# Performance work log

Hardware: AMD Instinct MI355X
Metric: run time of the kernel (lower is better)

Reference implementation:

```python
import jax, jax.numpy as jnp
import numpy as np

B, S, D = 4, 2048, 1024
H = 16
DK = D // H  # 64

def setup_inputs() -> dict:
    key = jax.random.key(0)
    ks = jax.random.split(key, 5)
    scale = 0.02
    return {
        "x": jax.random.normal(ks[0], (B, S, D), dtype=jnp.float32),
        "Wq": jax.random.normal(ks[1], (D, D), dtype=jnp.float32) * scale,
        "Wk": jax.random.normal(ks[2], (D, D), dtype=jnp.float32) * scale,
        "Wv": jax.random.normal(ks[3], (D, D), dtype=jnp.float32) * scale,
        "Wo": jax.random.normal(ks[4], (D, D), dtype=jnp.float32) * scale,
    }

def reference(x, Wq, Wk, Wv, Wo):
    b, s, d = x.shape
    h, dk = H, DK
    # torch nn.Linear(bias=False): y = x @ W.T
    q = (x @ Wq.T).reshape(b, s, h, dk).transpose(0, 2, 1, 3)  # [b,h,s,dk]
    k = (x @ Wk.T).reshape(b, s, h, dk).transpose(0, 2, 1, 3)
    v = (x @ Wv.T).reshape(b, s, h, dk).transpose(0, 2, 1, 3)
    scores = jnp.einsum('bhqd,bhkd->bhqk', q, k) * (dk ** -0.5)
    causal = jnp.triu(jnp.ones((s, s), dtype=bool), k=1)  # True = masked out
    scores = jnp.where(causal, -jnp.inf, scores)
    probs = jax.nn.softmax(scores, axis=-1)
    attn = jnp.einsum('bhqk,bhkd->bhqd', probs, v)  # [b,h,s,dk]
    attn = attn.transpose(0, 2, 1, 3).reshape(b, s, d)
    return attn @ Wo.T
```

## Files before the change

kernel.cpp:

```cpp
#include <hip/hip_runtime.h>

typedef __attribute__((ext_vector_type(8))) short bf16x8;
typedef __attribute__((ext_vector_type(4))) float f32x4;
typedef __attribute__((ext_vector_type(2))) unsigned int u32x2;
typedef unsigned int u32;
typedef unsigned short u16;

constexpr int Bb = 4, S = 2048, D = 1024, H = 16, DK = 64, M = Bb * S;

#if __has_builtin(__builtin_amdgcn_exp2f)
#define EXP2F __builtin_amdgcn_exp2f
#else
#define EXP2F exp2f
#endif

__device__ __forceinline__ u16 f2bf(float f) {
  u32 u = __float_as_uint(f);
  return (u16)((u + 0x7fffu + ((u >> 16) & 1u)) >> 16);
}

__device__ __forceinline__ u32 cvt_pk_bf16(float a, float b) {
  u32 r;
  asm("v_cvt_pk_bf16_f32 %0, %1, %2" : "=v"(r) : "v"(a), "v"(b));
  return r;
}

__device__ __forceinline__ void gld_lds16(const u16* g, u16* l) {
  __builtin_amdgcn_global_load_lds((const __attribute__((address_space(1))) u32*)g,
                                   (__attribute__((address_space(3))) u32*)l, 16, 0, 0);
}

__global__ void cast_kernel(const float* __restrict__ s, u16* __restrict__ d, int n) {
  int i = (blockIdx.x * blockDim.x + threadIdx.x) * 4;
  if (i >= n) return;
  float4 f = *(const float4*)(s + i);
  ushort4 o;
  o.x = f2bf(f.x); o.y = f2bf(f.y); o.z = f2bf(f.z); o.w = f2bf(f.w);
  *(ushort4*)(d + i) = o;
}

struct CastArgs { const float* s[4]; u16* d[4]; float sc[4]; };
__global__ void cast4_kernel(CastArgs a) {
  int i = (blockIdx.x * blockDim.x + threadIdx.x) * 4;
  int w = i >> 20;
  int off = i & ((1 << 20) - 1);
  float sc = a.sc[w];
  float4 f = *(const float4*)(a.s[w] + off);
  ushort4 o;
  o.x = f2bf(f.x * sc); o.y = f2bf(f.y * sc); o.z = f2bf(f.z * sc); o.w = f2bf(f.w * sc);
  *(ushort4*)(a.d[w] + off) = o;
}

template <bool OUTF32>
__device__ __forceinline__ void gemm_core(const u16* __restrict__ A,
                                          const u16* __restrict__ Bt,
                                          float* __restrict__ Cf, u16* __restrict__ Cb,
                                          int Nn, int Kk, int m0, int n0,
                                          u16* As, u16* Bs) {
  const int tid = threadIdx.x, wave = tid >> 6, lane = tid & 63;
  const int quad = lane >> 4, col = lane & 15;
  const int wm = wave >> 1, wn = wave & 1;

  f32x4 acc[4][4];
#pragma unroll
  for (int i = 0; i < 4; i++)
#pragma unroll
    for (int j = 0; j < 4; j++) acc[i][j] = (f32x4){0.f, 0.f, 0.f, 0.f};

  for (int k0 = 0; k0 < Kk; k0 += 64) {
#pragma unroll
    for (int j = 0; j < 4; j++) {
      int g = (wave * 4 + j) * 64;
      int gl = g + lane;
      int r = gl >> 3, sl = gl & 7;
      int kof = (sl ^ (r & 7)) * 8;
      const u16* ga = A + (size_t)(m0 + r) * Kk + k0 + kof;
      gld_lds16(ga, &As[g * 8]);
      const u16* gb = Bt + (size_t)(n0 + r) * Kk + k0 + kof;
      gld_lds16(gb, &Bs[g * 8]);
    }
    __syncthreads();
#pragma unroll
    for (int kb = 0; kb < 2; kb++) {
      bf16x8 af[4], bfr[4];
#pragma unroll
      for (int mi = 0; mi < 4; mi++) {
        int R = wm * 64 + mi * 16 + col;
        af[mi] = *(const bf16x8*)&As[R * 64 + (((kb * 4 + quad) ^ (R & 7)) << 3)];
      }
#pragma unroll
      for (int ni = 0; ni < 4; ni++) {
        int R = wn * 64 + ni * 16 + col;
        bfr[ni] = *(const bf16x8*)&Bs[R * 64 + (((kb * 4 + quad) ^ (R & 7)) << 3)];
      }
#pragma unroll
      for (int mi = 0; mi < 4; mi++)
#pragma unroll
        for (int ni = 0; ni < 4; ni++)
          acc[mi][ni] = __builtin_amdgcn_mfma_f32_16x16x32_bf16(af[mi], bfr[ni], acc[mi][ni], 0, 0, 0);
    }
    __syncthreads();
  }
#pragma unroll
  for (int mi = 0; mi < 4; mi++)
#pragma unroll
    for (int ni = 0; ni < 4; ni++)
#pragma unroll
      for (int r = 0; r < 4; r++) {
        int row = m0 + wm * 64 + mi * 16 + quad * 4 + r;
        int cc = n0 + wn * 64 + ni * 16 + col;
        float v = acc[mi][ni][r];
        if (OUTF32) Cf[(size_t)row * Nn + cc] = v;
        else Cb[(size_t)row * Nn + cc] = f2bf(v);
      }
}

struct QkvArgs { const u16* bt[3]; u16* c[3]; };
__global__ __launch_bounds__(256) void gemm_qkv(const u16* __restrict__ A, QkvArgs q) {
  __shared__ __align__(16) u16 As[128 * 64];
  __shared__ __align__(16) u16 Bs[128 * 64];
  int sel = blockIdx.x >> 3;
  int n0 = (blockIdx.x & 7) * 128, m0 = blockIdx.y * 128;
  gemm_core<false>(A, q.bt[sel], nullptr, q.c[sel], D, D, m0, n0, As, Bs);
}

__global__ __launch_bounds__(256) void gemm_f32(const u16* __restrict__ A,
                                                const u16* __restrict__ Bt,
                                                float* __restrict__ C) {
  __shared__ __align__(16) u16 As[128 * 64];
  __shared__ __align__(16) u16 Bs[128 * 64];
  gemm_core<true>(A, Bt, C, nullptr, D, D, blockIdx.y * 128, blockIdx.x * 128, As, Bs);
}

__global__ __launch_bounds__(256) void attn_kernel(const u16* __restrict__ Q,
                                                   const u16* __restrict__ K,
                                                   const u16* __restrict__ V,
                                                   u16* __restrict__ O) {
  __shared__ __align__(16) u16 Ks[2][2][64 * 32];
  __shared__ __align__(16) u16 Vt[2][64 * 64];
  __shared__ __align__(16) u16 Pw[4][32 * 64];
  const int tid = threadIdx.x, wave = tid >> 6, lane = tid & 63;
  const int quad = lane >> 4, col = lane & 15;
  const int bh = blockIdx.x, b = bh >> 4, h = bh & 15;
  const int qb = 15 - (int)blockIdx.y;
  const size_t base = (size_t)b * S * D + h * DK;

  const int vk0 = (tid & 31) * 2;
  const int vdg = tid >> 5;

  bf16x8 bones;
#pragma unroll
  for (int e = 0; e < 8; e++) bones[e] = (short)0x3F80;

  auto kdma = [&](int ktile, int buf) {
    int c = tid, cb = wave * 64;
    int kk = c >> 2;
    int dch = (c & 3) ^ ((kk >> 1) & 3);
    const u16* g0 = K + base + (size_t)(ktile * 64 + kk) * D + dch * 8;
    gld_lds16(g0, &Ks[buf][0][cb * 8]);
    gld_lds16(g0 + 32, &Ks[buf][1][cb * 8]);
  };

  const int qw = qb * 128 + wave * 32;
  const int nkt = 2 * qb + 2;

  bf16x8 aq[2][2];
#pragma unroll
  for (int mi = 0; mi < 2; mi++)
#pragma unroll
    for (int kb = 0; kb < 2; kb++)
      aq[mi][kb] = *(const bf16x8*)(Q + base + (size_t)(qw + mi * 16 + col) * D + kb * 32 + quad * 8);

  f32x4 ao[2][4], lacc[2];
#pragma unroll
  for (int mi = 0; mi < 2; mi++) {
    lacc[mi] = (f32x4){0.f, 0.f, 0.f, 0.f};
#pragma unroll
    for (int dg = 0; dg < 4; dg++) ao[mi][dg] = (f32x4){0.f, 0.f, 0.f, 0.f};
  }

  bf16x8 vA0, vA1, vB0, vB1;
  {
    const u16* vp = V + base + (size_t)vk0 * D + vdg * 8;
    vA0 = *(const bf16x8*)vp; vA1 = *(const bf16x8*)(vp + D);
  }
  kdma(0, 0);
  auto vstage = [&](int buf, bf16x8 r0, bf16x8 r1) {
    int kgrp = vk0 >> 3, kin = vk0 & 7;
#pragma unroll
    for (int e = 0; e < 8; e++) {
      u32 val = ((u32)(u16)r0[e]) | ((u32)(u16)r1[e] << 16);
      int slot = (kgrp ^ e) & 7;
      *(u32*)&Vt[buf][(vdg * 8 + e) * 64 + (slot << 3) + kin] = val;
    }
  };
  vstage(0, vA0, vA1);
  {
    const u16* vp = V + base + (size_t)(64 + vk0) * D + vdg * 8;
    vB0 = *(const bf16x8*)vp; vB1 = *(const bf16x8*)(vp + D);
  }

  for (int kt = 0; kt < nkt; kt++) {
    const int bf = kt & 1, nb = bf ^ 1, ph = kt & 1;
    __syncthreads();
    const bool active = (kt * 64 <= qw + 31);
    if (kt + 1 < nkt) {
      kdma(kt + 1, nb);
      vstage(nb, ph ? vA0 : vB0, ph ? vA1 : vB1);
      if (kt + 2 < nkt) {
        const u16* vp = V + base + (size_t)((kt + 2) * 64 + vk0) * D + vdg * 8;
        if (ph) { vB0 = *(const bf16x8*)vp; vB1 = *(const bf16x8*)(vp + D); }
        else    { vA0 = *(const bf16x8*)vp; vA1 = *(const bf16x8*)(vp + D); }
      }
    }
    if (!active) continue;
    bf16x8 bk0[4], bk1[4];
    const int ksl = ((quad ^ ((col >> 1) & 3)) & 3) << 3;
#pragma unroll
    for (int n16 = 0; n16 < 4; n16++) {
      bk0[n16] = *(const bf16x8*)&Ks[bf][0][(n16 * 16 + col) * 32 + ksl];
      bk1[n16] = *(const bf16x8*)&Ks[bf][1][(n16 * 16 + col) * 32 + ksl];
    }
    f32x4 sacc[2][4];
#pragma unroll
    for (int qi = 0; qi < 2; qi++)
#pragma unroll
      for (int n16 = 0; n16 < 4; n16++) sacc[qi][n16] = (f32x4){0.f, 0.f, 0.f, 0.f};
    __builtin_amdgcn_s_setprio(1);
#pragma unroll
    for (int qi = 0; qi < 2; qi++)
#pragma unroll
      for (int n16 = 0; n16 < 4; n16++) {
        sacc[qi][n16] = __builtin_amdgcn_mfma_f32_16x16x32_bf16(bk0[n16], aq[qi][0], sacc[qi][n16], 0, 0, 0);
        sacc[qi][n16] = __builtin_amdgcn_mfma_f32_16x16x32_bf16(bk1[n16], aq[qi][1], sacc[qi][n16], 0, 0, 0);
      }
    __builtin_amdgcn_s_setprio(0);
    const bool full = (kt * 64 + 63) <= qw;
#pragma unroll
    for (int qi = 0; qi < 2; qi++) {
      const int row = qi * 16 + col;
      const int rsw = row & 7;
      const int qg = qw + row;
#pragma unroll
      for (int n16 = 0; n16 < 4; n16++) {
        float p0 = EXP2F(sacc[qi][n16][0]);
        float p1 = EXP2F(sacc[qi][n16][1]);
        float p2 = EXP2F(sacc[qi][n16][2]);
        float p3 = EXP2F(sacc[qi][n16][3]);
        if (!full) {
          int kg = kt * 64 + n16 * 16 + quad * 4;
          p0 = (kg + 0 > qg) ? 0.f : p0;
          p1 = (kg + 1 > qg) ? 0.f : p1;
          p2 = (kg + 2 > qg) ? 0.f : p2;
          p3 = (kg + 3 > qg) ? 0.f : p3;
        }
        u32 lo = cvt_pk_bf16(p0, p1);
        u32 hi = cvt_pk_bf16(p2, p3);
        int slot = ((n16 * 2 + (quad >> 1)) ^ rsw) & 7;
        *(u32x2*)&Pw[wave][row * 64 + (slot << 3) + ((quad & 1) << 2)] = (u32x2){lo, hi};
      }
    }
    bf16x8 bv[2][4];
#pragma unroll
    for (int kb = 0; kb < 2; kb++)
#pragma unroll
      for (int dg = 0; dg < 4; dg++)
        bv[kb][dg] = *(const bf16x8*)&Vt[bf][(dg * 16 + col) * 64 + ((((kb * 4 + quad) ^ (col & 7)) & 7) << 3)];
#pragma unroll
    for (int mi = 0; mi < 2; mi++) {
      const int row = mi * 16 + col;
      const int rsw = row & 7;
      bf16x8 ap0 = *(const bf16x8*)&Pw[wave][row * 64 + (((quad ^ rsw) & 7) << 3)];
      bf16x8 ap1 = *(const bf16x8*)&Pw[wave][row * 64 + ((((4 + quad) ^ rsw) & 7) << 3)];
      __builtin_amdgcn_s_setprio(1);
#pragma unroll
      for (int dg = 0; dg < 4; dg++) {
        ao[mi][dg] = __builtin_amdgcn_mfma_f32_16x16x32_bf16(ap0, bv[0][dg], ao[mi][dg], 0, 0, 0);
        ao[mi][dg] = __builtin_amdgcn_mfma_f32_16x16x32_bf16(ap1, bv[1][dg], ao[mi][dg], 0, 0, 0);
      }
      lacc[mi] = __builtin_amdgcn_mfma_f32_16x16x32_bf16(ap0, bones, lacc[mi], 0, 0, 0);
      lacc[mi] = __builtin_amdgcn_mfma_f32_16x16x32_bf16(ap1, bones, lacc[mi], 0, 0, 0);
      __builtin_amdgcn_s_setprio(0);
    }
  }
#pragma unroll
  for (int mi = 0; mi < 2; mi++)
#pragma unroll
    for (int r = 0; r < 4; r++) {
      float inv = 1.f / lacc[mi][r];
      int q = qw + mi * 16 + quad * 4 + r;
#pragma unroll
      for (int dg = 0; dg < 4; dg++)
        O[base + (size_t)q * D + dg * 16 + col] = f2bf(ao[mi][dg][r] * inv);
    }
}

extern "C" void kernel_launch(void* const* d_in, const int* in_sizes, int n_in,
                              void* d_out, int out_size, void* d_ws, size_t ws_size,
                              hipStream_t stream) {
  const float* x  = (const float*)d_in[0];
  const float* Wq = (const float*)d_in[1];
  const float* Wk = (const float*)d_in[2];
  const float* Wv = (const float*)d_in[3];
  const float* Wo = (const float*)d_in[4];

  u16* xb  = (u16*)d_ws;
  u16* wqb = xb + (size_t)M * D;
  u16* wkb = wqb + (size_t)D * D;
  u16* wvb = wkb + (size_t)D * D;
  u16* wob = wvb + (size_t)D * D;
  u16* Qb  = wob + (size_t)D * D;
  u16* Kb  = Qb + (size_t)M * D;
  u16* Vb  = Kb + (size_t)M * D;
  u16* Ab  = xb;

  cast_kernel<<<M * D / 1024, 256, 0, stream>>>(x, xb, M * D);
  CastArgs ca;
  ca.s[0] = Wq; ca.s[1] = Wk; ca.s[2] = Wv; ca.s[3] = Wo;
  ca.d[0] = wqb; ca.d[1] = wkb; ca.d[2] = wvb; ca.d[3] = wob;
  ca.sc[0] = 0.18033688011112042f;
  ca.sc[1] = 1.f; ca.sc[2] = 1.f; ca.sc[3] = 1.f;
  cast4_kernel<<<4 * D * D / 1024, 256, 0, stream>>>(ca);

  QkvArgs qa;
  qa.bt[0] = wqb; qa.bt[1] = wkb; qa.bt[2] = wvb;
  qa.c[0] = Qb; qa.c[1] = Kb; qa.c[2] = Vb;
  gemm_qkv<<<dim3(24, M / 128), 256, 0, stream>>>(xb, qa);

  attn_kernel<<<dim3(Bb * H, 16), 256, 0, stream>>>(Qb, Kb, Vb, Ab);

  gemm_f32<<<dim3(D / 128, M / 128), 256, 0, stream>>>(Ab, wob, (float*)d_out);
}
```

Measured before the change: 267.0 us.

## Keep softmax probabilities in registers and use 16x16x16 MFMA for PV

The attention kernel no longer stages the bf16 probability tile through a per-wave LDS buffer. The QK^T accumulator layout is reused directly as the A operand of 16x16x16 bf16 MFMAs for the PV product and the row-sum. This removes the LDS write and readback plus the Pw buffer, cutting LDS footprint, and the launch bounds now request 4 blocks per CU. In exchange it issues twice as many smaller-K MFMAs with lower per-instruction throughput, and V is read in 8-byte chunks instead of 16-byte ones.

```diff
diff --git a/kernel.cpp b/kernel.cpp
--- a/kernel.cpp
+++ b/kernel.cpp
@@ -1,8 +1,8 @@
 #include <hip/hip_runtime.h>
 
 typedef __attribute__((ext_vector_type(8))) short bf16x8;
+typedef __attribute__((ext_vector_type(4))) short bf16x4;
 typedef __attribute__((ext_vector_type(4))) float f32x4;
-typedef __attribute__((ext_vector_type(2))) unsigned int u32x2;
 typedef unsigned int u32;
 typedef unsigned short u16;
 
@@ -23,6 +23,15 @@
   u32 r;
   asm("v_cvt_pk_bf16_f32 %0, %1, %2" : "=v"(r) : "v"(a), "v"(b));
   return r;
+}
+
+__device__ __forceinline__ f32x4 mfma16(bf16x4 a, bf16x4 b, f32x4 c) {
+#if __has_builtin(__builtin_amdgcn_mfma_f32_16x16x16bf16_1k)
+  return __builtin_amdgcn_mfma_f32_16x16x16bf16_1k(a, b, c, 0, 0, 0);
+#else
+  asm("v_mfma_f32_16x16x16_bf16 %0, %1, %2, %0" : "+v"(c) : "v"(a), "v"(b));
+  return c;
+#endif
 }
 
 __device__ __forceinline__ void gld_lds16(const u16* g, u16* l) {
@@ -132,13 +141,12 @@
   gemm_core<true>(A, Bt, C, nullptr, D, D, blockIdx.y * 128, blockIdx.x * 128, As, Bs);
 }
 
-__global__ __launch_bounds__(256) void attn_kernel(const u16* __restrict__ Q,
-                                                   const u16* __restrict__ K,
-                                                   const u16* __restrict__ V,
-                                                   u16* __restrict__ O) {
+__global__ __launch_bounds__(256, 4) void attn_kernel(const u16* __restrict__ Q,
+                                                      const u16* __restrict__ K,
+                                                      const u16* __restrict__ V,
+                                                      u16* __restrict__ O) {
   __shared__ __align__(16) u16 Ks[2][2][64 * 32];
   __shared__ __align__(16) u16 Vt[2][64 * 64];
-  __shared__ __align__(16) u16 Pw[4][32 * 64];
   const int tid = threadIdx.x, wave = tid >> 6, lane = tid & 63;
   const int quad = lane >> 4, col = lane & 15;
   const int bh = blockIdx.x, b = bh >> 4, h = bh & 15;
@@ -148,9 +156,9 @@
   const int vk0 = (tid & 31) * 2;
   const int vdg = tid >> 5;
 
-  bf16x8 bones;
-#pragma unroll
-  for (int e = 0; e < 8; e++) bones[e] = (short)0x3F80;
+  bf16x4 bones4;
+#pragma unroll
+  for (int e = 0; e < 4; e++) bones4[e] = (short)0x3F80;
 
   auto kdma = [&](int ktile, int buf) {
     int c = tid, cb = wave * 64;
@@ -236,11 +244,10 @@
       }
     __builtin_amdgcn_s_setprio(0);
     const bool full = (kt * 64 + 63) <= qw;
+    bf16x4 ap[2][4];
 #pragma unroll
     for (int qi = 0; qi < 2; qi++) {
-      const int row = qi * 16 + col;
-      const int rsw = row & 7;
-      const int qg = qw + row;
+      const int qg = qw + qi * 16 + col;
 #pragma unroll
       for (int n16 = 0; n16 < 4; n16++) {
         float p0 = EXP2F(sacc[qi][n16][0]);
@@ -254,32 +261,28 @@
           p2 = (kg + 2 > qg) ? 0.f : p2;
           p3 = (kg + 3 > qg) ? 0.f : p3;
         }
-        u32 lo = cvt_pk_bf16(p0, p1);
-        u32 hi = cvt_pk_bf16(p2, p3);
-        int slot = ((n16 * 2 + (quad >> 1)) ^ rsw) & 7;
-        *(u32x2*)&Pw[wave][row * 64 + (slot << 3) + ((quad & 1) << 2)] = (u32x2){lo, hi};
-      }
-    }
-    bf16x8 bv[2][4];
-#pragma unroll
-    for (int kb = 0; kb < 2; kb++)
+        union { u32 u[2]; bf16x4 v; } pk;
+        pk.u[0] = cvt_pk_bf16(p0, p1);
+        pk.u[1] = cvt_pk_bf16(p2, p3);
+        ap[qi][n16] = pk.v;
+      }
+    }
+#pragma unroll
+    for (int n16 = 0; n16 < 4; n16++) {
+      bf16x4 bv[4];
+      const int shalf = ((quad & 1) << 2);
+      const int sl = ((2 * n16 + (quad >> 1)) ^ (col & 7)) & 7;
 #pragma unroll
       for (int dg = 0; dg < 4; dg++)
-        bv[kb][dg] = *(const bf16x8*)&Vt[bf][(dg * 16 + col) * 64 + ((((kb * 4 + quad) ^ (col & 7)) & 7) << 3)];
-#pragma unroll
-    for (int mi = 0; mi < 2; mi++) {
-      const int row = mi * 16 + col;
-      const int rsw = row & 7;
-      bf16x8 ap0 = *(const bf16x8*)&Pw[wave][row * 64 + (((quad ^ rsw) & 7) << 3)];
-      bf16x8 ap1 = *(const bf16x8*)&Pw[wave][row * 64 + ((((4 + quad) ^ rsw) & 7) << 3)];
+        bv[dg] = *(const bf16x4*)&Vt[bf][(dg * 16 + col) * 64 + (sl << 3) + shalf];
       __builtin_amdgcn_s_setprio(1);
 #pragma unroll
-      for (int dg = 0; dg < 4; dg++) {
-        ao[mi][dg] = __builtin_amdgcn_mfma_f32_16x16x32_bf16(ap0, bv[0][dg], ao[mi][dg], 0, 0, 0);
-        ao[mi][dg] = __builtin_amdgcn_mfma_f32_16x16x32_bf16(ap1, bv[1][dg], ao[mi][dg], 0, 0, 0);
-      }
-      lacc[mi] = __builtin_amdgcn_mfma_f32_16x16x32_bf16(ap0, bones, lacc[mi], 0, 0, 0);
-      lacc[mi] = __builtin_amdgcn_mfma_f32_16x16x32_bf16(ap1, bones, lacc[mi], 0, 0, 0);
+      for (int mi = 0; mi < 2; mi++) {
+#pragma unroll
+        for (int dg = 0; dg < 4; dg++)
+          ao[mi][dg] = mfma16(ap[mi][n16], bv[dg], ao[mi][dg]);
+        lacc[mi] = mfma16(ap[mi][n16], bones4, lacc[mi]);
+      }
       __builtin_amdgcn_s_setprio(0);
     }
   }
```

After: 354.9 us. 32.9% more time.

## Pair causal query blocks per workgroup for balanced attention work

Applied to the files above, without the earlier changes.

Each attention workgroup now handles two 64-row query blocks, a long one (31-pi) and a short one (pi), run one after the other. Each wave therefore owns 16 query rows instead of 32, and every workgroup gets an equal number of key tiles under the causal mask. This is meant to remove the tail imbalance between short and long causal blocks. In exchange, K and V tiles are streamed twice per workgroup and each wave does less MFMA work per loaded tile, which lowers data reuse.

```diff
diff --git a/kernel.cpp b/kernel.cpp
--- a/kernel.cpp
+++ b/kernel.cpp
@@ -138,11 +138,11 @@
                                                    u16* __restrict__ O) {
   __shared__ __align__(16) u16 Ks[2][2][64 * 32];
   __shared__ __align__(16) u16 Vt[2][64 * 64];
-  __shared__ __align__(16) u16 Pw[4][32 * 64];
+  __shared__ __align__(16) u16 Pw[4][16 * 64];
   const int tid = threadIdx.x, wave = tid >> 6, lane = tid & 63;
   const int quad = lane >> 4, col = lane & 15;
   const int bh = blockIdx.x, b = bh >> 4, h = bh & 15;
-  const int qb = 15 - (int)blockIdx.y;
+  const int pi = blockIdx.y;
   const size_t base = (size_t)b * S * D + h * DK;
 
   const int vk0 = (tid & 31) * 2;
@@ -160,31 +160,6 @@
     gld_lds16(g0, &Ks[buf][0][cb * 8]);
     gld_lds16(g0 + 32, &Ks[buf][1][cb * 8]);
   };
-
-  const int qw = qb * 128 + wave * 32;
-  const int nkt = 2 * qb + 2;
-
-  bf16x8 aq[2][2];
-#pragma unroll
-  for (int mi = 0; mi < 2; mi++)
-#pragma unroll
-    for (int kb = 0; kb < 2; kb++)
-      aq[mi][kb] = *(const bf16x8*)(Q + base + (size_t)(qw + mi * 16 + col) * D + kb * 32 + quad * 8);
-
-  f32x4 ao[2][4], lacc[2];
-#pragma unroll
-  for (int mi = 0; mi < 2; mi++) {
-    lacc[mi] = (f32x4){0.f, 0.f, 0.f, 0.f};
-#pragma unroll
-    for (int dg = 0; dg < 4; dg++) ao[mi][dg] = (f32x4){0.f, 0.f, 0.f, 0.f};
-  }
-
-  bf16x8 vA0, vA1, vB0, vB1;
-  {
-    const u16* vp = V + base + (size_t)vk0 * D + vdg * 8;
-    vA0 = *(const bf16x8*)vp; vA1 = *(const bf16x8*)(vp + D);
-  }
-  kdma(0, 0);
   auto vstage = [&](int buf, bf16x8 r0, bf16x8 r1) {
     int kgrp = vk0 >> 3, kin = vk0 & 7;
 #pragma unroll
@@ -194,105 +169,119 @@
       *(u32*)&Vt[buf][(vdg * 8 + e) * 64 + (slot << 3) + kin] = val;
     }
   };
-  vstage(0, vA0, vA1);
-  {
-    const u16* vp = V + base + (size_t)(64 + vk0) * D + vdg * 8;
-    vB0 = *(const bf16x8*)vp; vB1 = *(const bf16x8*)(vp + D);
+
+  for (int half = 0; half < 2; half++) {
+    const int qsub = half ? pi : 31 - pi;
+    const int qw = qsub * 64 + wave * 16;
+    const int nkt = qsub + 1;
+
+    bf16x8 aq[2];
+#pragma unroll
+    for (int kb = 0; kb < 2; kb++)
+      aq[kb] = *(const bf16x8*)(Q + base + (size_t)(qw + col) * D + kb * 32 + quad * 8);
+
+    f32x4 ao[4], lacc;
+    lacc = (f32x4){0.f, 0.f, 0.f, 0.f};
+#pragma unroll
+    for (int dg = 0; dg < 4; dg++) ao[dg] = (f32x4){0.f, 0.f, 0.f, 0.f};
+
+    bf16x8 vA0, vA1, vB0, vB1;
+    {
+      const u16* vp = V + base + (size_t)vk0 * D + vdg * 8;
+      vA0 = *(const bf16x8*)vp; vA1 = *(const bf16x8*)(vp + D);
+    }
+    __syncthreads();
+    kdma(0, 0);
+    vstage(0, vA0, vA1);
+    {
+      const u16* vp = V + base + (size_t)(64 + vk0) * D + vdg * 8;
+      vB0 = *(const bf16x8*)vp; vB1 = *(const bf16x8*)(vp + D);
+    }
+
+    for (int kt = 0; kt < nkt; kt++) {
+      const int bf = kt & 1, nb = bf ^ 1, ph = kt & 1;
+      __syncthreads();
+      const bool active = (kt * 64 <= qw + 15);
+      if (kt + 1 < nkt) {
+        kdma(kt + 1, nb);
+        vstage(nb, ph ? vA0 : vB0, ph ? vA1 : vB1);
+        if (kt + 2 < nkt) {
+          const u16* vp = V + base + (size_t)((kt + 2) * 64 + vk0) * D + vdg * 8;
+          if (ph) { vB0 = *(const bf16x8*)vp; vB1 = *(const bf16x8*)(vp + D); }
+          else    { vA0 = *(const bf16x8*)vp; vA1 = *(const bf16x8*)(vp + D); }
+        }
+      }
+      if (!active) continue;
+      bf16x8 bk0[4], bk1[4];
+      const int ksl = ((quad ^ ((col >> 1) & 3)) & 3) << 3;
+#pragma unroll
+      for (int n16 = 0; n16 < 4; n16++) {
+        bk0[n16] = *(const bf16x8*)&Ks[bf][0][(n16 * 16 + col) * 32 + ksl];
+        bk1[n16] = *(const bf16x8*)&Ks[bf][1][(n16 * 16 + col) * 32 + ksl];
+      }
+      f32x4 sacc[4];
+#pragma unroll
+      for (int n16 = 0; n16 < 4; n16++) sacc[n16] = (f32x4){0.f, 0.f, 0.f, 0.f};
+      __builtin_amdgcn_s_setprio(1);
+#pragma unroll
+      for (int n16 = 0; n16 < 4; n16++) {
+        sacc[n16] = __builtin_amdgcn_mfma_f32_16x16x32_bf16(bk0[n16], aq[0], sacc[n16], 0, 0, 0);
+        sacc[n16] = __builtin_amdgcn_mfma_f32_16x16x32_bf16(bk1[n16], aq[1], sacc[n16], 0, 0, 0);
+      }
+      __builtin_amdgcn_s_setprio(0);
+      const bool full = (kt * 64 + 63) <= qw;
+      {
+        const int rsw = col & 7;
+        const int qg = qw + col;
+#pragma unroll
+        for (int n16 = 0; n16 < 4; n16++) {
+          float p0 = EXP2F(sacc[n16][0]);
+          float p1 = EXP2F(sacc[n16][1]);
+          float p2 = EXP2F(sacc[n16][2]);
+          float p3 = EXP2F(sacc[n16][3]);
+          if (!full) {
+            int kg = kt * 64 + n16 * 16 + quad * 4;
+            p0 = (kg + 0 > qg) ? 0.f : p0;
+            p1 = (kg + 1 > qg) ? 0.f : p1;
+            p2 = (kg + 2 > qg) ? 0.f : p2;
+            p3 = (kg + 3 > qg) ? 0.f : p3;
+          }
+          u32 lo = cvt_pk_bf16(p0, p1);
+          u32 hi = cvt_pk_bf16(p2, p3);
+          int slot = ((n16 * 2 + (quad >> 1)) ^ rsw) & 7;
+          *(u32x2*)&Pw[wave][col * 64 + (slot << 3) + ((quad & 1) << 2)] = (u32x2){lo, hi};
+        }
+      }
+      bf16x8 bv[2][4];
+#pragma unroll
+      for (int kb = 0; kb < 2; kb++)
+#pragma unroll
+        for (int dg = 0; dg < 4; dg++)
+          bv[kb][dg] = *(const bf16x8*)&Vt[bf][(dg * 16 + col) * 64 + ((((kb * 4 + quad) ^ (col & 7)) & 7) << 3)];
+      {
+        const int rsw = col & 7;
+        bf16x8 ap0 = *(const bf16x8*)&Pw[wave][col * 64 + (((quad ^ rsw) & 7) << 3)];
+        bf16x8 ap1 = *(const bf16x8*)&Pw[wave][col * 64 + ((((4 + quad) ^ rsw) & 7) << 3)];
+        __builtin_amdgcn_s_setprio(1);
+#pragma unroll
+        for (int dg = 0; dg < 4; dg++) {
+          ao[dg] = __builtin_amdgcn_mfma_f32_16x16x32_bf16(ap0, bv[0][dg], ao[dg], 0, 0, 0);
+          ao[dg] = __builtin_amdgcn_mfma_f32_16x16x32_bf16(ap1, bv[1][dg], ao[dg], 0, 0, 0);
+        }
+        lacc = __builtin_amdgcn_mfma_f32_16x16x32_bf16(ap0, bones, lacc, 0, 0, 0);
+        lacc = __builtin_amdgcn_mfma_f32_16x16x32_bf16(ap1, bones, lacc, 0, 0, 0);
+        __builtin_amdgcn_s_setprio(0);
+      }
+    }
+#pragma unroll
+    for (int r = 0; r < 4; r++) {
+      float inv = 1.f / lacc[r];
+      int q = qw + quad * 4 + r;
+#pragma unroll
+      for (int dg = 0; dg < 4; dg++)
+        O[base + (size_t)q * D + dg * 16 + col] = f2bf(ao[dg][r] * inv);
+    }
   }
-
-  for (int kt = 0; kt < nkt; kt++) {
-    const int bf = kt & 1, nb = bf ^ 1, ph = kt & 1;
-    __syncthreads();
-    const bool active = (kt * 64 <= qw + 31);
-    if (kt + 1 < nkt) {
-      kdma(kt + 1, nb);
-      vstage(nb, ph ? vA0 : vB0, ph ? vA1 : vB1);
-      if (kt + 2 < nkt) {
-        const u16* vp = V + base + (size_t)((kt + 2) * 64 + vk0) * D + vdg * 8;
-        if (ph) { vB0 = *(const bf16x8*)vp; vB1 = *(const bf16x8*)(vp + D); }
-        else    { vA0 = *(const bf16x8*)vp; vA1 = *(const bf16x8*)(vp + D); }
-      }
-    }
-    if (!active) continue;
-    bf16x8 bk0[4], bk1[4];
-    const int ksl = ((quad ^ ((col >> 1) & 3)) & 3) << 3;
-#pragma unroll
-    for (int n16 = 0; n16 < 4; n16++) {
-      bk0[n16] = *(const bf16x8*)&Ks[bf][0][(n16 * 16 + col) * 32 + ksl];
-      bk1[n16] = *(const bf16x8*)&Ks[bf][1][(n16 * 16 + col) * 32 + ksl];
-    }
-    f32x4 sacc[2][4];
-#pragma unroll
-    for (int qi = 0; qi < 2; qi++)
-#pragma unroll
-      for (int n16 = 0; n16 < 4; n16++) sacc[qi][n16] = (f32x4){0.f, 0.f, 0.f, 0.f};
-    __builtin_amdgcn_s_setprio(1);
-#pragma unroll
-    for (int qi = 0; qi < 2; qi++)
-#pragma unroll
-      for (int n16 = 0; n16 < 4; n16++) {
-        sacc[qi][n16] = __builtin_amdgcn_mfma_f32_16x16x32_bf16(bk0[n16], aq[qi][0], sacc[qi][n16], 0, 0, 0);
-        sacc[qi][n16] = __builtin_amdgcn_mfma_f32_16x16x32_bf16(bk1[n16], aq[qi][1], sacc[qi][n16], 0, 0, 0);
-      }
-    __builtin_amdgcn_s_setprio(0);
-    const bool full = (kt * 64 + 63) <= qw;
-#pragma unroll
-    for (int qi = 0; qi < 2; qi++) {
-      const int row = qi * 16 + col;
-      const int rsw = row & 7;
-      const int qg = qw + row;
-#pragma unroll
-      for (int n16 = 0; n16 < 4; n16++) {
-        float p0 = EXP2F(sacc[qi][n16][0]);
-        float p1 = EXP2F(sacc[qi][n16][1]);
-        float p2 = EXP2F(sacc[qi][n16][2]);
-        float p3 = EXP2F(sacc[qi][n16][3]);
-        if (!full) {
-          int kg = kt * 64 + n16 * 16 + quad * 4;
-          p0 = (kg + 0 > qg) ? 0.f : p0;
-          p1 = (kg + 1 > qg) ? 0.f : p1;
-          p2 = (kg + 2 > qg) ? 0.f : p2;
-          p3 = (kg + 3 > qg) ? 0.f : p3;
-        }
-        u32 lo = cvt_pk_bf16(p0, p1);
-        u32 hi = cvt_pk_bf16(p2, p3);
-        int slot = ((n16 * 2 + (quad >> 1)) ^ rsw) & 7;
-        *(u32x2*)&Pw[wave][row * 64 + (slot << 3) + ((quad & 1) << 2)] = (u32x2){lo, hi};
-      }
-    }
-    bf16x8 bv[2][4];
-#pragma unroll
-    for (int kb = 0; kb < 2; kb++)
-#pragma unroll
-      for (int dg = 0; dg < 4; dg++)
-        bv[kb][dg] = *(const bf16x8*)&Vt[bf][(dg * 16 + col) * 64 + ((((kb * 4 + quad) ^ (col & 7)) & 7) << 3)];
-#pragma unroll
-    for (int mi = 0; mi < 2; mi++) {
-      const int row = mi * 16 + col;
-      const int rsw = row & 7;
-      bf16x8 ap0 = *(const bf16x8*)&Pw[wave][row * 64 + (((quad ^ rsw) & 7) << 3)];
-      bf16x8 ap1 = *(const bf16x8*)&Pw[wave][row * 64 + ((((4 + quad) ^ rsw) & 7) << 3)];
-      __builtin_amdgcn_s_setprio(1);
-#pragma unroll
-      for (int dg = 0; dg < 4; dg++) {
-        ao[mi][dg] = __builtin_amdgcn_mfma_f32_16x16x32_bf16(ap0, bv[0][dg], ao[mi][dg], 0, 0, 0);
-        ao[mi][dg] = __builtin_amdgcn_mfma_f32_16x16x32_bf16(ap1, bv[1][dg], ao[mi][dg], 0, 0, 0);
-      }
-      lacc[mi] = __builtin_amdgcn_mfma_f32_16x16x32_bf16(ap0, bones, lacc[mi], 0, 0, 0);
-      lacc[mi] = __builtin_amdgcn_mfma_f32_16x16x32_bf16(ap1, bones, lacc[mi], 0, 0, 0);
-      __builtin_amdgcn_s_setprio(0);
-    }
-  }
-#pragma unroll
-  for (int mi = 0; mi < 2; mi++)
-#pragma unroll
-    for (int r = 0; r < 4; r++) {
-      float inv = 1.f / lacc[mi][r];
-      int q = qw + mi * 16 + quad * 4 + r;
-#pragma unroll
-      for (int dg = 0; dg < 4; dg++)
-        O[base + (size_t)q * D + dg * 16 + col] = f2bf(ao[mi][dg][r] * inv);
-    }
 }
 
 extern "C" void kernel_launch(void* const* d_in, const int* in_sizes, int n_in,
```

New measurement: 276.5 us. 1.04x slower.

## Pair causal query blocks per workgroup and unroll K-loop by two buffers

Applied to the files above, without the earlier changes.

Each attention workgroup now handles two query blocks (qb and 15-qb) in sequence, so every block does the same amount of causal work and the grid shrinks from 1024 to 512 workgroups. The K/V tile loop is manually unrolled by two so buffer indices are compile-time constants, and LDS addresses and swizzle offsets are precomputed outside the loop. This targets tail imbalance from the triangular workload and per-iteration address arithmetic. In exchange there are fewer workgroups to fill the CUs and more live registers per thread.

```diff
diff --git a/kernel.cpp b/kernel.cpp
--- a/kernel.cpp
+++ b/kernel.cpp
@@ -142,7 +142,7 @@
   const int tid = threadIdx.x, wave = tid >> 6, lane = tid & 63;
   const int quad = lane >> 4, col = lane & 15;
   const int bh = blockIdx.x, b = bh >> 4, h = bh & 15;
-  const int qb = 15 - (int)blockIdx.y;
+  const int pair = blockIdx.y;
   const size_t base = (size_t)b * S * D + h * DK;
 
   const int vk0 = (tid & 31) * 2;
@@ -152,147 +152,182 @@
 #pragma unroll
   for (int e = 0; e < 8; e++) bones[e] = (short)0x3F80;
 
-  auto kdma = [&](int ktile, int buf) {
-    int c = tid, cb = wave * 64;
-    int kk = c >> 2;
-    int dch = (c & 3) ^ ((kk >> 1) & 3);
-    const u16* g0 = K + base + (size_t)(ktile * 64 + kk) * D + dch * 8;
-    gld_lds16(g0, &Ks[buf][0][cb * 8]);
-    gld_lds16(g0 + 32, &Ks[buf][1][cb * 8]);
-  };
-
-  const int qw = qb * 128 + wave * 32;
-  const int nkt = 2 * qb + 2;
-
-  bf16x8 aq[2][2];
-#pragma unroll
-  for (int mi = 0; mi < 2; mi++)
-#pragma unroll
-    for (int kb = 0; kb < 2; kb++)
-      aq[mi][kb] = *(const bf16x8*)(Q + base + (size_t)(qw + mi * 16 + col) * D + kb * 32 + quad * 8);
-
-  f32x4 ao[2][4], lacc[2];
-#pragma unroll
-  for (int mi = 0; mi < 2; mi++) {
-    lacc[mi] = (f32x4){0.f, 0.f, 0.f, 0.f};
-#pragma unroll
-    for (int dg = 0; dg < 4; dg++) ao[mi][dg] = (f32x4){0.f, 0.f, 0.f, 0.f};
-  }
-
-  bf16x8 vA0, vA1, vB0, vB1;
-  {
-    const u16* vp = V + base + (size_t)vk0 * D + vdg * 8;
-    vA0 = *(const bf16x8*)vp; vA1 = *(const bf16x8*)(vp + D);
-  }
-  kdma(0, 0);
-  auto vstage = [&](int buf, bf16x8 r0, bf16x8 r1) {
-    int kgrp = vk0 >> 3, kin = vk0 & 7;
+  const int rsw = col & 7;
+  const int ksl = ((quad ^ ((col >> 1) & 3)) & 3) << 3;
+  const u16* kbase[2] = { &Ks[0][0][col * 32 + ksl], &Ks[1][0][col * 32 + ksl] };
+  const int vsl0 = ((quad ^ rsw) & 7) << 3;
+  const int vsl1 = (((4 + quad) ^ rsw) & 7) << 3;
+  const u16* vbase[2] = { &Vt[0][col * 64], &Vt[1][col * 64] };
+  u16* pww[2] = { &Pw[wave][col * 64 + (quad & 1) * 4],
+                  &Pw[wave][(16 + col) * 64 + (quad & 1) * 4] };
+  int swof[4];
+#pragma unroll
+  for (int n16 = 0; n16 < 4; n16++)
+    swof[n16] = (((n16 * 2 + (quad >> 1)) ^ rsw) & 7) << 3;
+  const u16* apbase[2] = { &Pw[wave][col * 64], &Pw[wave][(16 + col) * 64] };
+  const int kk = tid >> 2;
+  const int dch = (tid & 3) ^ ((kk >> 1) & 3);
+  const int cb = wave * 64;
+  u16* dk[2][2] = { { &Ks[0][0][cb * 8], &Ks[0][1][cb * 8] },
+                    { &Ks[1][0][cb * 8], &Ks[1][1][cb * 8] } };
+  const int kgrp = vk0 >> 3, kin = vk0 & 7;
+  u16* vwb[2] = { &Vt[0][vdg * 8 * 64 + kin], &Vt[1][vdg * 8 * 64 + kin] };
+  int vwof[8];
+#pragma unroll
+  for (int e = 0; e < 8; e++) vwof[e] = e * 64 + ((kgrp ^ e) & 7) * 8;
+
+  auto vstage = [&](const int buf, bf16x8 r0, bf16x8 r1) {
+    u16* wb = vwb[buf];
 #pragma unroll
     for (int e = 0; e < 8; e++) {
       u32 val = ((u32)(u16)r0[e]) | ((u32)(u16)r1[e] << 16);
-      int slot = (kgrp ^ e) & 7;
-      *(u32*)&Vt[buf][(vdg * 8 + e) * 64 + (slot << 3) + kin] = val;
+      *(u32*)(wb + vwof[e]) = val;
     }
   };
-  vstage(0, vA0, vA1);
-  {
-    const u16* vp = V + base + (size_t)(64 + vk0) * D + vdg * 8;
-    vB0 = *(const bf16x8*)vp; vB1 = *(const bf16x8*)(vp + D);
+
+  for (int half = 0; half < 2; half++) {
+    const int qb = half ? pair : 15 - pair;
+    const int qw = qb * 128 + wave * 32;
+    const int nkt = 2 * qb + 2;
+
+    bf16x8 aq[2][2];
+#pragma unroll
+    for (int mi = 0; mi < 2; mi++)
+#pragma unroll
+      for (int kb = 0; kb < 2; kb++)
+        aq[mi][kb] = *(const bf16x8*)(Q + base + (size_t)(qw + mi * 16 + col) * D + kb * 32 + quad * 8);
+
+    f32x4 ao[2][4], lacc[2];
+#pragma unroll
+    for (int mi = 0; mi < 2; mi++) {
+      lacc[mi] = (f32x4){0.f, 0.f, 0.f, 0.f};
+#pragma unroll
+      for (int dg = 0; dg < 4; dg++) ao[mi][dg] = (f32x4){0.f, 0.f, 0.f, 0.f};
+    }
+
+    auto compute = [&](const int BF, int kt) {
+      const u16* kbK = kbase[BF];
+      bf16x8 bk0[4], bk1[4];
+#pragma unroll
+      for (int n16 = 0; n16 < 4; n16++) {
+        bk0[n16] = *(const bf16x8*)(kbK + n16 * 512);
+        bk1[n16] = *(const bf16x8*)(kbK + n16 * 512 + 2048);
+      }
+      f32x4 sacc[2][4];
+#pragma unroll
+      for (int qi = 0; qi < 2; qi++)
+#pragma unroll
+        for (int n16 = 0; n16 < 4; n16++) sacc[qi][n16] = (f32x4){0.f, 0.f, 0.f, 0.f};
+      __builtin_amdgcn_s_setprio(1);
+#pragma unroll
+      for (int qi = 0; qi < 2; qi++)
+#pragma unroll
+        for (int n16 = 0; n16 < 4; n16++) {
+          sacc[qi][n16] = __builtin_amdgcn_mfma_f32_16x16x32_bf16(bk0[n16], aq[qi][0], sacc[qi][n16], 0, 0, 0);
+          sacc[qi][n16] = __builtin_amdgcn_mfma_f32_16x16x32_bf16(bk1[n16], aq[qi][1], sacc[qi][n16], 0, 0, 0);
+        }
+      __builtin_amdgcn_s_setprio(0);
+      const bool full = (kt * 64 + 63) <= qw;
+#pragma unroll
+      for (int qi = 0; qi < 2; qi++) {
+        const int qg = qw + qi * 16 + col;
+#pragma unroll
+        for (int n16 = 0; n16 < 4; n16++) {
+          float p0 = EXP2F(sacc[qi][n16][0]);
+          float p1 = EXP2F(sacc[qi][n16][1]);
+          float p2 = EXP2F(sacc[qi][n16][2]);
+          float p3 = EXP2F(sacc[qi][n16][3]);
+          if (!full) {
+            int kg = kt * 64 + n16 * 16 + quad * 4;
+            p0 = (kg + 0 > qg) ? 0.f : p0;
+            p1 = (kg + 1 > qg) ? 0.f : p1;
+            p2 = (kg + 2 > qg) ? 0.f : p2;
+            p3 = (kg + 3 > qg) ? 0.f : p3;
+          }
+          u32 lo = cvt_pk_bf16(p0, p1);
+          u32 hi = cvt_pk_bf16(p2, p3);
+          *(u32x2*)(pww[qi] + swof[n16]) = (u32x2){lo, hi};
+        }
+      }
+      const u16* vtB = vbase[BF];
+      bf16x8 bv0[4], bv1[4];
+#pragma unroll
+      for (int dg = 0; dg < 4; dg++) {
+        bv0[dg] = *(const bf16x8*)(vtB + dg * 1024 + vsl0);
+        bv1[dg] = *(const bf16x8*)(vtB + dg * 1024 + vsl1);
+      }
+#pragma unroll
+      for (int mi = 0; mi < 2; mi++) {
+        bf16x8 ap0 = *(const bf16x8*)(apbase[mi] + vsl0);
+        bf16x8 ap1 = *(const bf16x8*)(apbase[mi] + vsl1);
+        __builtin_amdgcn_s_setprio(1);
+#pragma unroll
+        for (int dg = 0; dg < 4; dg++) {
+          ao[mi][dg] = __builtin_amdgcn_mfma_f32_16x16x32_bf16(ap0, bv0[dg], ao[mi][dg], 0, 0, 0);
+          ao[mi][dg] = __builtin_amdgcn_mfma_f32_16x16x32_bf16(ap1, bv1[dg], ao[mi][dg], 0, 0, 0);
+        }
+        lacc[mi] = __builtin_amdgcn_mfma_f32_16x16x32_bf16(ap0, bones, lacc[mi], 0, 0, 0);
+        lacc[mi] = __builtin_amdgcn_mfma_f32_16x16x32_bf16(ap1, bones, lacc[mi], 0, 0, 0);
+        __builtin_amdgcn_s_setprio(0);
+      }
+    };
+
+    bf16x8 vA0, vA1, vB0, vB1;
+    const u16* gv = V + base + (size_t)vk0 * D + vdg * 8;
+    vA0 = *(const bf16x8*)gv;
+    vA1 = *(const bf16x8*)(gv + D);
+    __syncthreads();
+    const u16* gk = K + base + (size_t)kk * D + dch * 8;
+    gld_lds16(gk, dk[0][0]);
+    gld_lds16(gk + 32, dk[0][1]);
+    gk += (size_t)64 * D;
+    vstage(0, vA0, vA1);
+    vB0 = *(const bf16x8*)(gv + (size_t)64 * D);
+    vB1 = *(const bf16x8*)(gv + (size_t)64 * D + D);
+    gv += (size_t)128 * D;
+
+    for (int kt = 0; kt < nkt; kt += 2) {
+      __syncthreads();
+      {
+        gld_lds16(gk, dk[1][0]);
+        gld_lds16(gk + 32, dk[1][1]);
+        gk += (size_t)64 * D;
+        vstage(1, vB0, vB1);
+        if (kt + 2 < nkt) {
+          vA0 = *(const bf16x8*)gv;
+          vA1 = *(const bf16x8*)(gv + D);
+          gv += (size_t)64 * D;
+        }
+        if (kt * 64 <= qw + 31) compute(0, kt);
+      }
+      __syncthreads();
+      {
+        const int kt1 = kt + 1;
+        if (kt1 + 1 < nkt) {
+          gld_lds16(gk, dk[0][0]);
+          gld_lds16(gk + 32, dk[0][1]);
+          gk += (size_t)64 * D;
+          vstage(0, vA0, vA1);
+          if (kt1 + 2 < nkt) {
+            vB0 = *(const bf16x8*)gv;
+            vB1 = *(const bf16x8*)(gv + D);
+            gv += (size_t)64 * D;
+          }
+        }
+        if (kt1 * 64 <= qw + 31) compute(1, kt1);
+      }
+    }
+#pragma unroll
+    for (int mi = 0; mi < 2; mi++)
+#pragma unroll
+      for (int r = 0; r < 4; r++) {
+        float inv = 1.f / lacc[mi][r];
+        int q = qw + mi * 16 + quad * 4 + r;
+#pragma unroll
+        for (int dg = 0; dg < 4; dg++)
+          O[base + (size_t)q * D + dg * 16 + col] = f2bf(ao[mi][dg][r] * inv);
+      }
   }
-
-  for (int kt = 0; kt < nkt; kt++) {
-    const int bf = kt & 1, nb = bf ^ 1, ph = kt & 1;
-    __syncthreads();
-    const bool active = (kt * 64 <= qw + 31);
-    if (kt + 1 < nkt) {
-      kdma(kt + 1, nb);
-      vstage(nb, ph ? vA0 : vB0, ph ? vA1 : vB1);
-      if (kt + 2 < nkt) {
-        const u16* vp = V + base + (size_t)((kt + 2) * 64 + vk0) * D + vdg * 8;
-        if (ph) { vB0 = *(const bf16x8*)vp; vB1 = *(const bf16x8*)(vp + D); }
-        else    { vA0 = *(const bf16x8*)vp; vA1 = *(const bf16x8*)(vp + D); }
-      }
-    }
-    if (!active) continue;
-    bf16x8 bk0[4], bk1[4];
-    const int ksl = ((quad ^ ((col >> 1) & 3)) & 3) << 3;
-#pragma unroll
-    for (int n16 = 0; n16 < 4; n16++) {
-      bk0[n16] = *(const bf16x8*)&Ks[bf][0][(n16 * 16 + col) * 32 + ksl];
-      bk1[n16] = *(const bf16x8*)&Ks[bf][1][(n16 * 16 + col) * 32 + ksl];
-    }
-    f32x4 sacc[2][4];
-#pragma unroll
-    for (int qi = 0; qi < 2; qi++)
-#pragma unroll
-      for (int n16 = 0; n16 < 4; n16++) sacc[qi][n16] = (f32x4){0.f, 0.f, 0.f, 0.f};
-    __builtin_amdgcn_s_setprio(1);
-#pragma unroll
-    for (int qi = 0; qi < 2; qi++)
-#pragma unroll
-      for (int n16 = 0; n16 < 4; n16++) {
-        sacc[qi][n16] = __builtin_amdgcn_mfma_f32_16x16x32_bf16(bk0[n16], aq[qi][0], sacc[qi][n16], 0, 0, 0);
-        sacc[qi][n16] = __builtin_amdgcn_mfma_f32_16x16x32_bf16(bk1[n16], aq[qi][1], sacc[qi][n16], 0, 0, 0);
-      }
-    __builtin_amdgcn_s_setprio(0);
-    const bool full = (kt * 64 + 63) <= qw;
-#pragma unroll
-    for (int qi = 0; qi < 2; qi++) {
-      const int row = qi * 16 + col;
-      const int rsw = row & 7;
-      const int qg = qw + row;
-#pragma unroll
-      for (int n16 = 0; n16 < 4; n16++) {
-        float p0 = EXP2F(sacc[qi][n16][0]);
-        float p1 = EXP2F(sacc[qi][n16][1]);
-        float p2 = EXP2F(sacc[qi][n16][2]);
-        float p3 = EXP2F(sacc[qi][n16][3]);
-        if (!full) {
-          int kg = kt * 64 + n16 * 16 + quad * 4;
-          p0 = (kg + 0 > qg) ? 0.f : p0;
-          p1 = (kg + 1 > qg) ? 0.f : p1;
-          p2 = (kg + 2 > qg) ? 0.f : p2;
-          p3 = (kg + 3 > qg) ? 0.f : p3;
-        }
-        u32 lo = cvt_pk_bf16(p0, p1);
-        u32 hi = cvt_pk_bf16(p2, p3);
-        int slot = ((n16 * 2 + (quad >> 1)) ^ rsw) & 7;
-        *(u32x2*)&Pw[wave][row * 64 + (slot << 3) + ((quad & 1) << 2)] = (u32x2){lo, hi};
-      }
-    }
-    bf16x8 bv[2][4];
-#pragma unroll
-    for (int kb = 0; kb < 2; kb++)
-#pragma unroll
-      for (int dg = 0; dg < 4; dg++)
-        bv[kb][dg] = *(const bf16x8*)&Vt[bf][(dg * 16 + col) * 64 + ((((kb * 4 + quad) ^ (col & 7)) & 7) << 3)];
-#pragma unroll
-    for (int mi = 0; mi < 2; mi++) {
-      const int row = mi * 16 + col;
-      const int rsw = row & 7;
-      bf16x8 ap0 = *(const bf16x8*)&Pw[wave][row * 64 + (((quad ^ rsw) & 7) << 3)];
-      bf16x8 ap1 = *(const bf16x8*)&Pw[wave][row * 64 + ((((4 + quad) ^ rsw) & 7) << 3)];
-      __builtin_amdgcn_s_setprio(1);
-#pragma unroll
-      for (int dg = 0; dg < 4; dg++) {
-        ao[mi][dg] = __builtin_amdgcn_mfma_f32_16x16x32_bf16(ap0, bv[0][dg], ao[mi][dg], 0, 0, 0);
-        ao[mi][dg] = __builtin_amdgcn_mfma_f32_16x16x32_bf16(ap1, bv[1][dg], ao[mi][dg], 0, 0, 0);
-      }
-      lacc[mi] = __builtin_amdgcn_mfma_f32_16x16x32_bf16(ap0, bones, lacc[mi], 0, 0, 0);
-      lacc[mi] = __builtin_amdgcn_mfma_f32_16x16x32_bf16(ap1, bones, lacc[mi], 0, 0, 0);
-      __builtin_amdgcn_s_setprio(0);
-    }
-  }
-#pragma unroll
-  for (int mi = 0; mi < 2; mi++)
-#pragma unroll
-    for (int r = 0; r < 4; r++) {
-      float inv = 1.f / lacc[mi][r];
-      int q = qw + mi * 16 + quad * 4 + r;
-#pragma unroll
-      for (int dg = 0; dg < 4; dg++)
-        O[base + (size_t)q * D + dg * 16 + col] = f2bf(ao[mi][dg][r] * inv);
-    }
 }
 
 extern "C" void kernel_launch(void* const* d_in, const int* in_sizes, int n_in,
@@ -327,7 +362,7 @@
   qa.c[0] = Qb; qa.c[1] = Kb; qa.c[2] = Vb;
   gemm_qkv<<<dim3(24, M / 128), 256, 0, stream>>>(xb, qa);
 
-  attn_kernel<<<dim3(Bb * H, 16), 256, 0, stream>>>(Qb, Kb, Vb, Ab);
+  attn_kernel<<<dim3(Bb * H, 8), 256, 0, stream>>>(Qb, Kb, Vb, Ab);
 
   gemm_f32<<<dim3(D / 128, M / 128), 256, 0, stream>>>(Ab, wob, (float*)d_out);
 }
```

Result: faster. 247.4 us (-7.3%).
